# Optimization experiments

Measured on AMD Instinct MI355X. Metric: run time of the kernel, lower is better.

The kernel has to match this reference:

```python
import jax, jax.numpy as jnp
import numpy as np

N_TOKENS = 16384  # b * seq_len
D_MODEL = 4096
NUM_EXPERTS = 64
TOP_K = 2
EPS = 1e-8


def setup_inputs() -> dict:
    key = jax.random.key(0)
    kx, kw = jax.random.split(key)
    x = jax.random.normal(kx, (N_TOKENS, D_MODEL), dtype=jnp.float32)
    # nn.Linear weight: [num_experts, d_model], scaled like torch default init
    W = jax.random.normal(kw, (NUM_EXPERTS, D_MODEL), dtype=jnp.float32) / jnp.sqrt(D_MODEL)
    return {"x": x, "W": W}


def reference(x, W):
    # logits: [n_tokens, num_experts]
    logits = jnp.einsum('nd,ed->ne', x, W)
    scores = jax.nn.softmax(logits, axis=-1)
    topk_scores, topk_indices = jax.lax.top_k(scores, TOP_K)
    topk_scores = topk_scores / jnp.sum(topk_scores, axis=-1, keepdims=True)
    expert_prob = jnp.mean(scores, axis=0)  # [num_experts]
    load_balancing_loss = jnp.sum(expert_prob * jnp.log(expert_prob + EPS))
    return topk_scores, topk_indices, load_balancing_loss
```

## Files before the change

### kernel.cpp

```cpp
#include <hip/hip_runtime.h>

#define NT 16384
#define DM 4096
#define NE 64
#define MB 64
#define KSPLIT 8
#define KW (DM / KSPLIT)
#define KSTEPS (KW / 32)

typedef __attribute__((ext_vector_type(8))) short bf16x8;
typedef __attribute__((ext_vector_type(4))) float f32x4;

__device__ __forceinline__ unsigned short bf16_rne(float f) {
  const unsigned u = __float_as_uint(f);
  return (unsigned short)((u + 0x7FFFu + ((u >> 16) & 1u)) >> 16);
}

__global__ void w_convert(const float* __restrict__ W,
                          unsigned short* __restrict__ Whi,
                          unsigned short* __restrict__ Wlo) {
  const int id   = blockIdx.x * 256 + threadIdx.x;
  const int lane = id & 63;
  const int nt   = (id >> 6) & 3;
  const int ks   = id >> 8;
  const float* src = W + (size_t)(nt * 16 + (lane & 15)) * DM + ks * 32 + (lane >> 4) * 8;
  unsigned short h[8], l[8];
#pragma unroll
  for (int j = 0; j < 8; ++j) {
    const float f = src[j];
    h[j] = bf16_rne(f);
    l[j] = bf16_rne(f - __uint_as_float((unsigned)h[j] << 16));
  }
  uint4 ph, pl;
  ph.x = h[0] | ((unsigned)h[1] << 16); ph.y = h[2] | ((unsigned)h[3] << 16);
  ph.z = h[4] | ((unsigned)h[5] << 16); ph.w = h[6] | ((unsigned)h[7] << 16);
  pl.x = l[0] | ((unsigned)l[1] << 16); pl.y = l[2] | ((unsigned)l[3] << 16);
  pl.z = l[4] | ((unsigned)l[5] << 16); pl.w = l[6] | ((unsigned)l[7] << 16);
  *(uint4*)(Whi + (size_t)id * 8) = ph;
  *(uint4*)(Wlo + (size_t)id * 8) = pl;
}

__launch_bounds__(512, 2)
__global__ void moe_mfma(const float* __restrict__ x,
                         const unsigned short* __restrict__ Whi,
                         const unsigned short* __restrict__ Wlo,
                         float* __restrict__ out,
                         float* __restrict__ bsum) {
  __shared__ float slab[8][8][66];
  __shared__ float esums[8][NE];

  const int tid  = threadIdx.x;
  const int lane = tid & 63;
  const int wv   = tid >> 6;
  const int wvu  = __builtin_amdgcn_readfirstlane(wv);
  const int blk  = blockIdx.x;

  const float* ap[4];
#pragma unroll
  for (int mt = 0; mt < 4; ++mt)
    ap[mt] = x + (size_t)(blk * MB + mt * 16 + (lane & 15)) * DM + wv * KW + (lane >> 4) * 8;

  const int ks0 = wv * KSTEPS;

  f32x4 acc[4][4];
#pragma unroll
  for (int mt = 0; mt < 4; ++mt)
#pragma unroll
    for (int nt = 0; nt < 4; ++nt) acc[mt][nt] = (f32x4){0.f, 0.f, 0.f, 0.f};

  float4 c0[4], c1[4];
#pragma unroll
  for (int mt = 0; mt < 4; ++mt) {
    c0[mt] = *(const float4*)(ap[mt]);
    c1[mt] = *(const float4*)(ap[mt] + 4);
  }

#pragma unroll 2
  for (int i = 0; i < KSTEPS; ++i) {
    float4 n0[4], n1[4];
    if (i + 1 < KSTEPS) {
#pragma unroll
      for (int mt = 0; mt < 4; ++mt) {
        n0[mt] = *(const float4*)(ap[mt] + (i + 1) * 32);
        n1[mt] = *(const float4*)(ap[mt] + (i + 1) * 32 + 4);
      }
    }
    const size_t fb = (size_t)(ks0 + i) * 4 * 512;
    bf16x8 bh[4], bl[4];
#pragma unroll
    for (int nt = 0; nt < 4; ++nt) {
      bh[nt] = *(const bf16x8*)(Whi + fb + nt * 512 + lane * 8);
      bl[nt] = *(const bf16x8*)(Wlo + fb + nt * 512 + lane * 8);
    }
    bf16x8 ah[4], al[4];
#pragma unroll
    for (int mt = 0; mt < 4; ++mt) {
      float fr[8];
      fr[0] = c0[mt].x; fr[1] = c0[mt].y; fr[2] = c0[mt].z; fr[3] = c0[mt].w;
      fr[4] = c1[mt].x; fr[5] = c1[mt].y; fr[6] = c1[mt].z; fr[7] = c1[mt].w;
#pragma unroll
      for (int j = 0; j < 8; ++j) {
        const unsigned short hb = bf16_rne(fr[j]);
        ah[mt][j] = (short)hb;
        al[mt][j] = (short)bf16_rne(fr[j] - __uint_as_float((unsigned)hb << 16));
      }
    }
#pragma unroll
    for (int mt = 0; mt < 4; ++mt)
#pragma unroll
      for (int nt = 0; nt < 4; ++nt) {
        acc[mt][nt] = __builtin_amdgcn_mfma_f32_16x16x32_bf16(al[mt], bl[nt], acc[mt][nt], 0, 0, 0);
        acc[mt][nt] = __builtin_amdgcn_mfma_f32_16x16x32_bf16(al[mt], bh[nt], acc[mt][nt], 0, 0, 0);
        acc[mt][nt] = __builtin_amdgcn_mfma_f32_16x16x32_bf16(ah[mt], bl[nt], acc[mt][nt], 0, 0, 0);
        acc[mt][nt] = __builtin_amdgcn_mfma_f32_16x16x32_bf16(ah[mt], bh[nt], acc[mt][nt], 0, 0, 0);
      }
    if (i + 1 < KSTEPS) {
#pragma unroll
      for (int mt = 0; mt < 4; ++mt) { c0[mt] = n0[mt]; c1[mt] = n1[mt]; }
    }
  }

  float lg[8];
#pragma unroll
  for (int s = 0; s < 8; ++s) {
    const int mt = s >> 1, g = 2 * (s & 1);
    const int q = lane >> 4;
    if (q == g || q == g + 1) {
#pragma unroll
      for (int nt = 0; nt < 4; ++nt)
#pragma unroll
        for (int r = 0; r < 4; ++r)
          slab[wv][(q - g) * 4 + r][nt * 16 + (lane & 15)] = acc[mt][nt][r];
    }
    __syncthreads();
    if (wvu == s) {
#pragma unroll
      for (int t = 0; t < 8; ++t) {
        float v = 0.f;
#pragma unroll
        for (int w = 0; w < 8; ++w) v += slab[w][t][lane];
        lg[t] = v;
      }
    }
    __syncthreads();
  }

  float esum = 0.f;
#pragma unroll
  for (int ti = 0; ti < 8; ++ti) {
    const float lgv = lg[ti];
    float m = lgv;
#pragma unroll
    for (int off = 32; off; off >>= 1) m = fmaxf(m, __shfl_xor(m, off, 64));
    const float p = __expf(lgv - m);
    float Z = p;
#pragma unroll
    for (int off = 32; off; off >>= 1) Z += __shfl_xor(Z, off, 64);
    const float s = p / Z;
    esum += s;

    float v1 = s; int i1 = lane;
#pragma unroll
    for (int off = 32; off; off >>= 1) {
      const float ov = __shfl_xor(v1, off, 64);
      const int   oi = __shfl_xor(i1, off, 64);
      if (ov > v1 || (ov == v1 && oi < i1)) { v1 = ov; i1 = oi; }
    }
    float sv = (lane == i1) ? -1.f : s;
    float v2 = sv; int i2 = lane;
#pragma unroll
    for (int off = 32; off; off >>= 1) {
      const float ov = __shfl_xor(v2, off, 64);
      const int   oi = __shfl_xor(i2, off, 64);
      if (ov > v2 || (ov == v2 && oi < i2)) { v2 = ov; i2 = oi; }
    }

    if (lane == 0) {
      const int gt = blk * MB + wvu * 8 + ti;
      const float inv = 1.f / (v1 + v2);
      out[2 * gt]              = v1 * inv;
      out[2 * gt + 1]          = v2 * inv;
      out[2 * NT + 2 * gt]     = (float)i1;
      out[2 * NT + 2 * gt + 1] = (float)i2;
    }
  }

  esums[wvu][lane] = esum;
  __syncthreads();
  if (wvu == 0) {
    float tot = 0.f;
#pragma unroll
    for (int w = 0; w < 8; ++w) tot += esums[w][lane];
    bsum[blk * NE + lane] = tot;
  }
}

__global__ void moe_gate_loss(const float* __restrict__ bsum,
                              float* __restrict__ out) {
  __shared__ float red[4][64];
  const int e = threadIdx.x & 63;
  const int g = threadIdx.x >> 6;
  float s = 0.f;
  for (int b = g; b < NT / MB; b += 4) s += bsum[b * 64 + e];
  red[g][e] = s;
  __syncthreads();
  if (threadIdx.x < 64) {
    const float tot = red[0][e] + red[1][e] + red[2][e] + red[3][e];
    const float p = tot * (1.f / (float)NT);
    float term = p * logf(p + 1e-8f);
#pragma unroll
    for (int off = 32; off; off >>= 1) term += __shfl_xor(term, off, 64);
    if (e == 0) out[4 * NT] = term;
  }
}

extern "C" void kernel_launch(void* const* d_in, const int* in_sizes, int n_in,
                              void* d_out, int out_size, void* d_ws, size_t ws_size,
                              hipStream_t stream) {
  const float* x = (const float*)d_in[0];
  const float* W = (const float*)d_in[1];
  float* out = (float*)d_out;

  unsigned short* Whi = (unsigned short*)d_ws;
  unsigned short* Wlo = Whi + (size_t)NE * DM;
  float* bsum = (float*)(Wlo + (size_t)NE * DM);

  hipLaunchKernelGGL(w_convert, dim3(128), dim3(256), 0, stream, W, Whi, Wlo);
  hipLaunchKernelGGL(moe_mfma, dim3(NT / MB), dim3(512), 0, stream, x, Whi, Wlo, out, bsum);
  hipLaunchKernelGGL(moe_gate_loss, dim3(1), dim3(256), 0, stream, bsum, out);
}
```

Before: 97.55 us.

## Shrink MFMA tile to 32 rows, 4-way K split, prefetch W fragments

Retiles the gating GEMM so each block handles 32 tokens with 4 waves splitting K, instead of 64 tokens with 8 waves. This gives 512 blocks of 256 threads, which should improve occupancy and load balance across CUs. The bf16 fragments of W are now double-buffered alongside x, and the fp32 to bf16 hi/lo split uses paired hardware conversion intrinsics. The trade-off is that each W fragment is reused across fewer token rows, so the weight traffic per token doubles.

```diff
diff --git a/kernel.cpp b/kernel.cpp
--- a/kernel.cpp
+++ b/kernel.cpp
@@ -1,10 +1,11 @@
 #include <hip/hip_runtime.h>
+#include <hip/hip_bf16.h>
 
 #define NT 16384
 #define DM 4096
 #define NE 64
-#define MB 64
-#define KSPLIT 8
+#define MB 32
+#define KSPLIT 4
 #define KW (DM / KSPLIT)
 #define KSTEPS (KW / 32)
 
@@ -14,6 +15,26 @@
 __device__ __forceinline__ unsigned short bf16_rne(float f) {
   const unsigned u = __float_as_uint(f);
   return (unsigned short)((u + 0x7FFFu + ((u >> 16) & 1u)) >> 16);
+}
+
+__device__ __forceinline__ void split2(float fa, float fb, unsigned& hp, unsigned& lp) {
+  union { __hip_bfloat162 h; unsigned u; } cv;
+  cv.h = __float22bfloat162_rn(make_float2(fa, fb));
+  hp = cv.u;
+  const float ha = __uint_as_float(hp << 16);
+  const float hb = __uint_as_float(hp & 0xFFFF0000u);
+  cv.h = __float22bfloat162_rn(make_float2(fa - ha, fb - hb));
+  lp = cv.u;
+}
+
+__device__ __forceinline__ void splitA(const float4& c0, const float4& c1,
+                                       bf16x8& hi, bf16x8& lo) {
+  union { unsigned u[4]; bf16x8 v; } H, L;
+  split2(c0.x, c0.y, H.u[0], L.u[0]);
+  split2(c0.z, c0.w, H.u[1], L.u[1]);
+  split2(c1.x, c1.y, H.u[2], L.u[2]);
+  split2(c1.z, c1.w, H.u[3], L.u[3]);
+  hi = H.v; lo = L.v;
 }
 
 __global__ void w_convert(const float* __restrict__ W,
@@ -40,14 +61,14 @@
   *(uint4*)(Wlo + (size_t)id * 8) = pl;
 }
 
-__launch_bounds__(512, 2)
+__launch_bounds__(256, 3)
 __global__ void moe_mfma(const float* __restrict__ x,
                          const unsigned short* __restrict__ Whi,
                          const unsigned short* __restrict__ Wlo,
                          float* __restrict__ out,
                          float* __restrict__ bsum) {
-  __shared__ float slab[8][8][66];
-  __shared__ float esums[8][NE];
+  __shared__ float slab[KSPLIT][8][66];
+  __shared__ float esums[4][NE];
 
   const int tid  = threadIdx.x;
   const int lane = tid & 63;
@@ -55,76 +76,75 @@
   const int wvu  = __builtin_amdgcn_readfirstlane(wv);
   const int blk  = blockIdx.x;
 
-  const float* ap[4];
-#pragma unroll
-  for (int mt = 0; mt < 4; ++mt)
-    ap[mt] = x + (size_t)(blk * MB + mt * 16 + (lane & 15)) * DM + wv * KW + (lane >> 4) * 8;
-
-  const int ks0 = wv * KSTEPS;
-
-  f32x4 acc[4][4];
-#pragma unroll
-  for (int mt = 0; mt < 4; ++mt)
+  const float* ap0 = x + (size_t)(blk * MB + (lane & 15)) * DM + wv * KW + (lane >> 4) * 8;
+  const float* ap1 = ap0 + (size_t)16 * DM;
+  const unsigned short* bh_p = Whi + (size_t)(wv * KSTEPS) * 2048 + lane * 8;
+  const unsigned short* bl_p = Wlo + (size_t)(wv * KSTEPS) * 2048 + lane * 8;
+
+  f32x4 acc[2][4];
+#pragma unroll
+  for (int mt = 0; mt < 2; ++mt)
 #pragma unroll
     for (int nt = 0; nt < 4; ++nt) acc[mt][nt] = (f32x4){0.f, 0.f, 0.f, 0.f};
 
-  float4 c0[4], c1[4];
-#pragma unroll
-  for (int mt = 0; mt < 4; ++mt) {
-    c0[mt] = *(const float4*)(ap[mt]);
-    c1[mt] = *(const float4*)(ap[mt] + 4);
+  float4 a00 = *(const float4*)(ap0);
+  float4 a01 = *(const float4*)(ap0 + 4);
+  float4 a10 = *(const float4*)(ap1);
+  float4 a11 = *(const float4*)(ap1 + 4);
+  bf16x8 bh[4], bl[4];
+#pragma unroll
+  for (int nt = 0; nt < 4; ++nt) {
+    bh[nt] = *(const bf16x8*)(bh_p + nt * 512);
+    bl[nt] = *(const bf16x8*)(bl_p + nt * 512);
   }
 
 #pragma unroll 2
   for (int i = 0; i < KSTEPS; ++i) {
-    float4 n0[4], n1[4];
+    float4 p00, p01, p10, p11;
+    bf16x8 nh[4], nl[4];
     if (i + 1 < KSTEPS) {
-#pragma unroll
-      for (int mt = 0; mt < 4; ++mt) {
-        n0[mt] = *(const float4*)(ap[mt] + (i + 1) * 32);
-        n1[mt] = *(const float4*)(ap[mt] + (i + 1) * 32 + 4);
+      const int o = (i + 1) * 32;
+      p00 = *(const float4*)(ap0 + o);
+      p01 = *(const float4*)(ap0 + o + 4);
+      p10 = *(const float4*)(ap1 + o);
+      p11 = *(const float4*)(ap1 + o + 4);
+      const size_t fb = (size_t)(i + 1) * 2048;
+#pragma unroll
+      for (int nt = 0; nt < 4; ++nt) {
+        nh[nt] = *(const bf16x8*)(bh_p + fb + nt * 512);
+        nl[nt] = *(const bf16x8*)(bl_p + fb + nt * 512);
       }
     }
-    const size_t fb = (size_t)(ks0 + i) * 4 * 512;
-    bf16x8 bh[4], bl[4];
+
+    bf16x8 ah0, al0, ah1, al1;
+    splitA(a00, a01, ah0, al0);
+    splitA(a10, a11, ah1, al1);
+
 #pragma unroll
     for (int nt = 0; nt < 4; ++nt) {
-      bh[nt] = *(const bf16x8*)(Whi + fb + nt * 512 + lane * 8);
-      bl[nt] = *(const bf16x8*)(Wlo + fb + nt * 512 + lane * 8);
-    }
-    bf16x8 ah[4], al[4];
-#pragma unroll
-    for (int mt = 0; mt < 4; ++mt) {
-      float fr[8];
-      fr[0] = c0[mt].x; fr[1] = c0[mt].y; fr[2] = c0[mt].z; fr[3] = c0[mt].w;
-      fr[4] = c1[mt].x; fr[5] = c1[mt].y; fr[6] = c1[mt].z; fr[7] = c1[mt].w;
-#pragma unroll
-      for (int j = 0; j < 8; ++j) {
-        const unsigned short hb = bf16_rne(fr[j]);
-        ah[mt][j] = (short)hb;
-        al[mt][j] = (short)bf16_rne(fr[j] - __uint_as_float((unsigned)hb << 16));
-      }
-    }
-#pragma unroll
-    for (int mt = 0; mt < 4; ++mt)
-#pragma unroll
-      for (int nt = 0; nt < 4; ++nt) {
-        acc[mt][nt] = __builtin_amdgcn_mfma_f32_16x16x32_bf16(al[mt], bl[nt], acc[mt][nt], 0, 0, 0);
-        acc[mt][nt] = __builtin_amdgcn_mfma_f32_16x16x32_bf16(al[mt], bh[nt], acc[mt][nt], 0, 0, 0);
-        acc[mt][nt] = __builtin_amdgcn_mfma_f32_16x16x32_bf16(ah[mt], bl[nt], acc[mt][nt], 0, 0, 0);
-        acc[mt][nt] = __builtin_amdgcn_mfma_f32_16x16x32_bf16(ah[mt], bh[nt], acc[mt][nt], 0, 0, 0);
-      }
+      acc[0][nt] = __builtin_amdgcn_mfma_f32_16x16x32_bf16(al0, bl[nt], acc[0][nt], 0, 0, 0);
+      acc[0][nt] = __builtin_amdgcn_mfma_f32_16x16x32_bf16(al0, bh[nt], acc[0][nt], 0, 0, 0);
+      acc[0][nt] = __builtin_amdgcn_mfma_f32_16x16x32_bf16(ah0, bl[nt], acc[0][nt], 0, 0, 0);
+      acc[0][nt] = __builtin_amdgcn_mfma_f32_16x16x32_bf16(ah0, bh[nt], acc[0][nt], 0, 0, 0);
+      acc[1][nt] = __builtin_amdgcn_mfma_f32_16x16x32_bf16(al1, bl[nt], acc[1][nt], 0, 0, 0);
+      acc[1][nt] = __builtin_amdgcn_mfma_f32_16x16x32_bf16(al1, bh[nt], acc[1][nt], 0, 0, 0);
+      acc[1][nt] = __builtin_amdgcn_mfma_f32_16x16x32_bf16(ah1, bl[nt], acc[1][nt], 0, 0, 0);
+      acc[1][nt] = __builtin_amdgcn_mfma_f32_16x16x32_bf16(ah1, bh[nt], acc[1][nt], 0, 0, 0);
+    }
+
     if (i + 1 < KSTEPS) {
-#pragma unroll
-      for (int mt = 0; mt < 4; ++mt) { c0[mt] = n0[mt]; c1[mt] = n1[mt]; }
+      a00 = p00; a01 = p01; a10 = p10; a11 = p11;
+#pragma unroll
+      for (int nt = 0; nt < 4; ++nt) { bh[nt] = nh[nt]; bl[nt] = nl[nt]; }
     }
   }
 
   float lg[8];
 #pragma unroll
-  for (int s = 0; s < 8; ++s) {
-    const int mt = s >> 1, g = 2 * (s & 1);
-    const int q = lane >> 4;
+  for (int s = 0; s < 4; ++s) {
+    const int mt = s >> 1;
+    const int g  = 2 * (s & 1);
+    const int q  = lane >> 4;
     if (q == g || q == g + 1) {
 #pragma unroll
       for (int nt = 0; nt < 4; ++nt)
@@ -138,7 +158,7 @@
       for (int t = 0; t < 8; ++t) {
         float v = 0.f;
 #pragma unroll
-        for (int w = 0; w < 8; ++w) v += slab[w][t][lane];
+        for (int w = 0; w < KSPLIT; ++w) v += slab[w][t][lane];
         lg[t] = v;
       }
     }
@@ -188,9 +208,7 @@
   esums[wvu][lane] = esum;
   __syncthreads();
   if (wvu == 0) {
-    float tot = 0.f;
-#pragma unroll
-    for (int w = 0; w < 8; ++w) tot += esums[w][lane];
+    float tot = esums[0][lane] + esums[1][lane] + esums[2][lane] + esums[3][lane];
     bsum[blk * NE + lane] = tot;
   }
 }
@@ -226,6 +244,6 @@
   float* bsum = (float*)(Wlo + (size_t)NE * DM);
 
   hipLaunchKernelGGL(w_convert, dim3(128), dim3(256), 0, stream, W, Whi, Wlo);
-  hipLaunchKernelGGL(moe_mfma, dim3(NT / MB), dim3(512), 0, stream, x, Whi, Wlo, out, bsum);
+  hipLaunchKernelGGL(moe_mfma, dim3(NT / MB), dim3(256), 0, stream, x, Whi, Wlo, out, bsum);
   hipLaunchKernelGGL(moe_gate_loss, dim3(1), dim3(256), 0, stream, bsum, out);
 }
```

Result: slower. 111.2 us (+14.0%).
